# Optimization experiments

Hardware: AMD Instinct MI355X
Metric: run time of the kernel (lower is better)

The kernel has to match this reference:

```python
import jax, jax.numpy as jnp
import numpy as np

DIM = 768
HEADS = 12
HEAD_DIM = DIM // HEADS
SCALE = HEAD_DIM ** (-0.5)


def setup_inputs() -> dict:
    key = jax.random.key(0)
    k1, k2, k3, k4 = jax.random.split(key, 4)
    B, N = 2, 48 * 48
    x = jax.random.normal(k1, (B, N, DIM), dtype=jnp.float32)
    qkv_w = jax.random.normal(k2, (3 * DIM, DIM), dtype=jnp.float32) * (DIM ** -0.5)
    proj_w = jax.random.normal(k3, (DIM, DIM), dtype=jnp.float32) * (DIM ** -0.5)
    proj_b = jax.random.normal(k4, (DIM,), dtype=jnp.float32) * 0.02
    return {"x": x, "H": 48, "W": 48, "qkv_w": qkv_w, "proj_w": proj_w, "proj_b": proj_b}


def reference(x, H, W, qkv_w, proj_w, proj_b):
    B, N, C = x.shape
    h, d = HEADS, HEAD_DIM
    # qkv linear (no bias): [B,N,3C], then split into per-head q,k,v [B,h,N,d]
    qkv = jnp.einsum('bnc,fc->bnf', x, qkv_w)
    qkv = qkv.reshape(B, N, 3, h, d).transpose(2, 0, 3, 1, 4)
    q, k, v = qkv[0], qkv[1], qkv[2]
    attn = jnp.einsum('bhnd,bhmd->bhnm', q, k) * SCALE  # [B,h,N,N]
    attn = jax.nn.softmax(attn, axis=-1)
    out = jnp.einsum('bhnm,bhmd->bhnd', attn, v)  # [B,h,N,d]
    out = out.transpose(0, 2, 1, 3).reshape(B, N, C)
    out = jnp.einsum('bnc,fc->bnf', out, proj_w) + proj_b
    return out
```

## Files before the change

kernel.cpp:

```cpp
#include <hip/hip_runtime.h>

#define B_    2
#define N_    2304
#define C_    768
#define HEADS 12
#define D_    64
#define F3    2304
#define M_    (B_*N_)
#define SPLITS 2
#define KSPAN (N_/SPLITS)
#define QSCALE 0.18033688011112042f

typedef __attribute__((ext_vector_type(8)))  short bfrag;
typedef __attribute__((ext_vector_type(4)))  float ffrag;
typedef __attribute__((ext_vector_type(16))) float ffrag16;
typedef __attribute__((ext_vector_type(4)))  unsigned ufrag;
typedef __attribute__((ext_vector_type(2)))  unsigned uint2v;

__device__ __forceinline__ short f2bf(float f) {
    unsigned u = __float_as_uint(f);
    u += 0x7fff + ((u >> 16) & 1);
    return (short)(u >> 16);
}

__device__ __forceinline__ void gl2lds16(const void* g, void* l) {
    __builtin_amdgcn_global_load_lds(
        (const __attribute__((address_space(1))) void*)g,
        (__attribute__((address_space(3))) void*)l, 16, 0, 0);
}

__device__ __forceinline__ void wait_vm8() { asm volatile("s_waitcnt vmcnt(8)" ::: "memory"); }
__device__ __forceinline__ void wait_vm4() { asm volatile("s_waitcnt vmcnt(4)" ::: "memory"); }
__device__ __forceinline__ void wait_vm0() { asm volatile("s_waitcnt vmcnt(0)" ::: "memory"); }

__device__ __forceinline__ unsigned pktrunc(float a, float b) {
    return __builtin_amdgcn_perm(__float_as_uint(a), __float_as_uint(b),
                                 0x03020706u);
}

__global__ __launch_bounds__(256) void cast_all(const float* __restrict__ x,
                                                const float* __restrict__ qw,
                                                const float* __restrict__ pw,
                                                short* __restrict__ dst) {
    const int nx4 = (M_*C_)/4, nq4 = (F3*C_)/4, np4 = (C_*C_)/4;
    int i = blockIdx.x * 256 + threadIdx.x;
    if (i >= nx4 + nq4 + np4) return;
    const float* src; int off;
    if (i < nx4)            { src = x;  off = i; }
    else if (i < nx4 + nq4) { src = qw; off = i - nx4; }
    else                    { src = pw; off = i - nx4 - nq4; }
    float4 v = ((const float4*)src)[off];
    short4 o;
    o.x = f2bf(v.x); o.y = f2bf(v.y); o.z = f2bf(v.z); o.w = f2bf(v.w);
    ((short4*)dst)[i] = o;
}

__global__ __launch_bounds__(256) void qkv_gemm(const short* __restrict__ xb,
                                                const short* __restrict__ wb,
                                                short* __restrict__ Qb,
                                                short* __restrict__ Kb,
                                                short* __restrict__ Vtb) {
    __shared__ short As[3][128*32];
    __shared__ short Bs[3][128*32];
    const int t = threadIdx.x;
    const int w = t >> 6, lane = t & 63;
    const int quad = lane >> 4, l15 = lane & 15;
    const int wr = w >> 1, wc = w & 1;

    const int nwg = gridDim.x * gridDim.y;
    const int bid = blockIdx.y * gridDim.x + blockIdx.x;
    const int swz = (bid & 7) * (nwg >> 3) + (bid >> 3);
    const int m0 = (swz / gridDim.x) * 128, f0 = (swz % gridDim.x) * 128;

    const int srow = lane >> 2;
    const int skk  = (lane & 3) * 8;

    ffrag acc[4][4] = {};

    #pragma unroll
    for (int r = 0; r < 2; ++r) {
        int seg = r*4 + w;
        int row = seg*16 + srow;
        gl2lds16(xb + (size_t)(m0+row)*C_ + skk, As[0] + seg*512);
        gl2lds16(wb + (size_t)(f0+row)*C_ + skk, Bs[0] + seg*512);
    }
    #pragma unroll
    for (int r = 0; r < 2; ++r) {
        int seg = r*4 + w;
        int row = seg*16 + srow;
        gl2lds16(xb + (size_t)(m0+row)*C_ + 32 + skk, As[1] + seg*512);
        gl2lds16(wb + (size_t)(f0+row)*C_ + 32 + skk, Bs[1] + seg*512);
    }

    const int NKT = C_/32;
    int cur = 0;
    for (int kt = 0; kt < NKT; ++kt) {
        int pf = cur + 2; if (pf >= 3) pf -= 3;
        if (kt + 2 < NKT) {
            const int k0n = (kt+2)*32;
            #pragma unroll
            for (int r = 0; r < 2; ++r) {
                int seg = r*4 + w;
                int row = seg*16 + srow;
                gl2lds16(xb + (size_t)(m0+row)*C_ + k0n + skk, As[pf] + seg*512);
                gl2lds16(wb + (size_t)(f0+row)*C_ + k0n + skk, Bs[pf] + seg*512);
            }
            wait_vm8();
        } else if (kt + 1 < NKT) {
            wait_vm4();
        } else {
            wait_vm0();
        }
        __builtin_amdgcn_s_barrier();

        bfrag af[4], bf[4];
        #pragma unroll
        for (int i = 0; i < 4; ++i)
            af[i] = *(const bfrag*)(As[cur] + (wr*64 + i*16 + l15)*32 + quad*8);
        #pragma unroll
        for (int j = 0; j < 4; ++j)
            bf[j] = *(const bfrag*)(Bs[cur] + (wc*64 + j*16 + l15)*32 + quad*8);
        #pragma unroll
        for (int i = 0; i < 4; ++i)
            #pragma unroll
            for (int j = 0; j < 4; ++j)
                acc[i][j] = __builtin_amdgcn_mfma_f32_16x16x32_bf16(af[i], bf[j], acc[i][j], 0, 0, 0);
        __builtin_amdgcn_s_barrier();
        cur = cur + 1; if (cur >= 3) cur = 0;
    }

    const int b   = m0 / N_;
    const int seg = f0 + wc*64;
    const int which = seg / C_;
    const int head  = (seg - which*C_) >> 6;
    const int bh    = b*HEADS + head;
    const int nbase = (m0 - b*N_) + wr*64 + quad*4;

    if (which == 0) {
        #pragma unroll
        for (int i = 0; i < 4; ++i) {
            int n0 = nbase + i*16;
            #pragma unroll
            for (int j = 0; j < 4; ++j) {
                int d = j*16 + l15;
                #pragma unroll
                for (int r = 0; r < 4; ++r)
                    Qb[((size_t)bh*N_ + n0 + r)*D_ + d] = f2bf(acc[i][j][r] * QSCALE);
            }
        }
    } else if (which == 1) {
        #pragma unroll
        for (int i = 0; i < 4; ++i) {
            int n0 = nbase + i*16;
            #pragma unroll
            for (int j = 0; j < 4; ++j) {
                int d = j*16 + l15;
                #pragma unroll
                for (int r = 0; r < 4; ++r)
                    Kb[((size_t)bh*N_ + n0 + r)*D_ + d] = f2bf(acc[i][j][r]);
            }
        }
    } else {
        #pragma unroll
        for (int i = 0; i < 4; ++i) {
            int n0 = nbase + i*16;
            #pragma unroll
            for (int j = 0; j < 4; ++j) {
                int d = j*16 + l15;
                short4 vv;
                vv.x = f2bf(acc[i][j][0]);
                vv.y = f2bf(acc[i][j][1]);
                vv.z = f2bf(acc[i][j][2]);
                vv.w = f2bf(acc[i][j][3]);
                *(short4*)(Vtb + ((size_t)bh*D_ + d)*N_ + n0) = vv;
            }
        }
    }
}


__device__ __forceinline__ void qkpack(const short* Kc, const bfrag* qf,
                                       int kt, int l31, int hi,
                                       ufrag& u0, ufrag& u1) {
    ffrag16 s;
    #pragma unroll
    for (int r = 0; r < 16; ++r) s[r] = 0.f;
    int row = kt*32 + l31, r7 = row & 7;
    __builtin_amdgcn_s_setprio(1);
    #pragma unroll
    for (int kc = 0; kc < 4; ++kc) {
        bfrag kf = *(const bfrag*)(Kc + row*64 + ((kc*2 + hi) ^ r7)*8);
        s = __builtin_amdgcn_mfma_f32_32x32x16_bf16(kf, qf[kc], s, 0, 0, 0);
    }
    __builtin_amdgcn_s_setprio(0);
    #pragma unroll
    for (int r = 0; r < 16; ++r)
        s[r] = __builtin_amdgcn_exp2f(s[r]);
    unsigned q01_0 = pktrunc(s[0],  s[1]),  q23_0 = pktrunc(s[2],  s[3]);
    unsigned q01_1 = pktrunc(s[4],  s[5]),  q23_1 = pktrunc(s[6],  s[7]);
    unsigned q01_2 = pktrunc(s[8],  s[9]),  q23_2 = pktrunc(s[10], s[11]);
    unsigned q01_3 = pktrunc(s[12], s[13]), q23_3 = pktrunc(s[14], s[15]);
    uint2v e0 = __builtin_amdgcn_permlane32_swap(q01_0, q01_1, false, false);
    uint2v e1 = __builtin_amdgcn_permlane32_swap(q23_0, q23_1, false, false);
    uint2v e2 = __builtin_amdgcn_permlane32_swap(q01_2, q01_3, false, false);
    uint2v e3 = __builtin_amdgcn_permlane32_swap(q23_2, q23_3, false, false);
    ufrag lo, hif;
    lo[0]  = e0[0]; lo[1]  = e1[0]; lo[2]  = e0[1]; lo[3]  = e1[1];
    hif[0] = e2[0]; hif[1] = e3[0]; hif[2] = e2[1]; hif[3] = e3[1];
    u0 = lo; u1 = hif;
}

__device__ __forceinline__ void pv_lds(ufrag u0, ufrag u1, const short* Vc,
                                       int kt, int l31, int hi, bfrag vones,
                                       ffrag16& o0, ffrag16& o1, ffrag16& lf) {
    int r0 = l31, r7a = r0 & 7;
    int r1 = 32 + l31, r7b = r1 & 7;
    bfrag p0 = __builtin_bit_cast(bfrag, u0);
    bfrag p1 = __builtin_bit_cast(bfrag, u1);
    int kcA = kt*2, kcB = kt*2 + 1;
    bfrag vA0 = *(const bfrag*)(Vc + r0*64 + ((kcA*2 + hi) ^ r7a)*8);
    bfrag vA1 = *(const bfrag*)(Vc + r1*64 + ((kcA*2 + hi) ^ r7b)*8);
    bfrag vB0 = *(const bfrag*)(Vc + r0*64 + ((kcB*2 + hi) ^ r7a)*8);
    bfrag vB1 = *(const bfrag*)(Vc + r1*64 + ((kcB*2 + hi) ^ r7b)*8);
    o0 = __builtin_amdgcn_mfma_f32_32x32x16_bf16(p0, vA0, o0, 0, 0, 0);
    o1 = __builtin_amdgcn_mfma_f32_32x32x16_bf16(p0, vA1, o1, 0, 0, 0);
    lf = __builtin_amdgcn_mfma_f32_32x32x16_bf16(p0, vones, lf, 0, 0, 0);
    o0 = __builtin_amdgcn_mfma_f32_32x32x16_bf16(p1, vB0, o0, 0, 0, 0);
    o1 = __builtin_amdgcn_mfma_f32_32x32x16_bf16(p1, vB1, o1, 0, 0, 0);
    lf = __builtin_amdgcn_mfma_f32_32x32x16_bf16(p1, vones, lf, 0, 0, 0);
}

__device__ __forceinline__ void pv_reg(ufrag u0, ufrag u1,
                                       bfrag v0, bfrag v1, bfrag v2, bfrag v3,
                                       bfrag vones,
                                       ffrag16& o0, ffrag16& o1, ffrag16& lf) {
    bfrag p0 = __builtin_bit_cast(bfrag, u0);
    bfrag p1 = __builtin_bit_cast(bfrag, u1);
    o0 = __builtin_amdgcn_mfma_f32_32x32x16_bf16(p0, v0, o0, 0, 0, 0);
    o1 = __builtin_amdgcn_mfma_f32_32x32x16_bf16(p0, v1, o1, 0, 0, 0);
    lf = __builtin_amdgcn_mfma_f32_32x32x16_bf16(p0, vones, lf, 0, 0, 0);
    o0 = __builtin_amdgcn_mfma_f32_32x32x16_bf16(p1, v2, o0, 0, 0, 0);
    o1 = __builtin_amdgcn_mfma_f32_32x32x16_bf16(p1, v3, o1, 0, 0, 0);
    lf = __builtin_amdgcn_mfma_f32_32x32x16_bf16(p1, vones, lf, 0, 0, 0);
}

__device__ __forceinline__ void vload4(const short* Vc, int kt, int l31, int hi,
                                       bfrag& v0, bfrag& v1, bfrag& v2, bfrag& v3) {
    int r0 = l31, r7a = r0 & 7;
    int r1 = 32 + l31, r7b = r1 & 7;
    int kcA = kt*2, kcB = kt*2 + 1;
    v0 = *(const bfrag*)(Vc + r0*64 + ((kcA*2 + hi) ^ r7a)*8);
    v1 = *(const bfrag*)(Vc + r1*64 + ((kcA*2 + hi) ^ r7b)*8);
    v2 = *(const bfrag*)(Vc + r0*64 + ((kcB*2 + hi) ^ r7a)*8);
    v3 = *(const bfrag*)(Vc + r1*64 + ((kcB*2 + hi) ^ r7b)*8);
}

__global__ __launch_bounds__(256, 4) void attn_mfma(const short* __restrict__ Qb,
                                                    const short* __restrict__ Kb,
                                                    const short* __restrict__ Vtb,
                                                    float* __restrict__ Opart,
                                                    float* __restrict__ lpart) {
    __shared__ short lds[16384];
    const int t = threadIdx.x;
    const int w = t >> 6, lane = t & 63;
    const int l31 = lane & 31, hi = lane >> 5;

    const int nwg = gridDim.x * gridDim.y;
    const int fid = blockIdx.y * gridDim.x + blockIdx.x;
    const int swz = (fid & 7) * (nwg >> 3) + (fid >> 3);
    const int bh  = swz / gridDim.x;
    const int q0  = (swz - bh * gridDim.x) * 128;

    const int split = blockIdx.z;
    const int kbase = split * KSPAN;
    const size_t base = (size_t)bh * N_ * D_;
    const int lrow = lane >> 3;
    const int lc   = (lane & 7) ^ lrow;

    short* Qs = lds + 8192;

    #pragma unroll
    for (int r = 0; r < 4; ++r) {
        int s = r*4 + w;
        gl2lds16(Qb + base + (size_t)(q0 + s*8 + lrow)*D_ + lc*8, Qs + s*512);
    }
    #pragma unroll
    for (int r = 0; r < 2; ++r) {
        int s = r*4 + w;
        int row = s*8 + lrow;
        gl2lds16(Kb  + base + (size_t)(kbase+row)*D_ + lc*8,    lds + s*512);
        gl2lds16(Vtb + (size_t)(bh*D_ + row)*N_ + kbase + lc*8, lds + 4096 + s*512);
    }
    __syncthreads();

    bfrag qf[4];
    {
        int row = w*32 + l31, r7 = row & 7;
        #pragma unroll
        for (int kc = 0; kc < 4; ++kc)
            qf[kc] = *(const bfrag*)(Qs + row*64 + ((kc*2 + hi) ^ r7)*8);
    }
    __syncthreads();

    bfrag vones;
    #pragma unroll
    for (int j = 0; j < 8; ++j) vones[j] = (short)0x3f80;

    ffrag16 oacc0, oacc1, lfr;
    #pragma unroll
    for (int r = 0; r < 16; ++r) { oacc0[r] = 0.f; oacc1[r] = 0.f; lfr[r] = 0.f; }

    const int NT = KSPAN / 64;

    ufrag pP0, pP1;
    bfrag vP0, vP1, vP2, vP3;

    {
        const int k0n = kbase + 64;
        #pragma unroll
        for (int r = 0; r < 2; ++r) {
            int s = r*4 + w;
            int row = s*8 + lrow;
            gl2lds16(Kb  + base + (size_t)(k0n+row)*D_ + lc*8,    lds + 8192 + s*512);
            gl2lds16(Vtb + (size_t)(bh*D_ + row)*N_ + k0n + lc*8, lds + 12288 + s*512);
        }
        const short* Kc = lds;
        const short* Vc = lds + 4096;
        ufrag a0, a1;
        qkpack(Kc, qf, 0, l31, hi, a0, a1);
        __builtin_amdgcn_s_setprio(1);
        pv_lds(a0, a1, Vc, 0, l31, hi, vones, oacc0, oacc1, lfr);
        __builtin_amdgcn_s_setprio(0);
        qkpack(Kc, qf, 1, l31, hi, pP0, pP1);
        vload4(Vc, 1, l31, hi, vP0, vP1, vP2, vP3);
        __builtin_amdgcn_s_barrier();
    }

    for (int ti = 1; ti < NT; ++ti) {
        const int cur = ti & 1;
        const short* Kc = lds + cur*8192;
        const short* Vc = Kc + 4096;

        if (ti + 1 < NT) {
            short* Kn = lds + (cur^1)*8192;
            const int k0n = kbase + (ti+1)*64;
            #pragma unroll
            for (int r = 0; r < 2; ++r) {
                int s = r*4 + w;
                int row = s*8 + lrow;
                gl2lds16(Kb  + base + (size_t)(k0n+row)*D_ + lc*8,    Kn + s*512);
                gl2lds16(Vtb + (size_t)(bh*D_ + row)*N_ + k0n + lc*8, Kn + 4096 + s*512);
            }
            wait_vm4();
        } else {
            wait_vm0();
        }
        __builtin_amdgcn_s_barrier();

        ufrag a0, a1;
        qkpack(Kc, qf, 0, l31, hi, a0, a1);
        __builtin_amdgcn_s_setprio(1);
        pv_reg(pP0, pP1, vP0, vP1, vP2, vP3, vones, oacc0, oacc1, lfr);
        pv_lds(a0, a1, Vc, 0, l31, hi, vones, oacc0, oacc1, lfr);
        __builtin_amdgcn_s_setprio(0);
        qkpack(Kc, qf, 1, l31, hi, pP0, pP1);
        vload4(Vc, 1, l31, hi, vP0, vP1, vP2, vP3);
        __builtin_amdgcn_s_barrier();
    }

    pv_reg(pP0, pP1, vP0, vP1, vP2, vP3, vones, oacc0, oacc1, lfr);

    const int b = bh / HEADS, head = bh - b*HEADS;
    float* Op = Opart + (size_t)split * M_ * C_;
    float* lp = lpart + (size_t)split * (B_*HEADS) * N_;

    if (l31 == 0) {
        #pragma unroll
        for (int r = 0; r < 16; ++r) {
            int n = q0 + w*32 + (r & 3) + 8*(r >> 2) + 4*hi;
            lp[bh*N_ + n] = lfr[r];
        }
    }

    #pragma unroll
    for (int r = 0; r < 16; ++r) {
        int n = q0 + w*32 + (r & 3) + 8*(r >> 2) + 4*hi;
        int c = head*D_ + l31;
        Op[((size_t)b*N_ + n)*C_ + c] = oacc0[r];
        Op[((size_t)b*N_ + n)*C_ + c + 32] = oacc1[r];
    }
}

__global__ __launch_bounds__(256) void attn_merge(const float* __restrict__ Opart,
                                                  const float* __restrict__ lpart,
                                                  short* __restrict__ Ob) {
    int i = blockIdx.x * 256 + threadIdx.x;
    int m = i / (C_/4);
    int c = (i - m*(C_/4)) * 4;
    int b = m / N_, n = m - b*N_;
    int bh = b*HEADS + (c >> 6);
    float4 o0 = ((const float4*)Opart)[i];
    float4 o1 = ((const float4*)(Opart + (size_t)M_*C_))[i];
    float l = lpart[bh*N_ + n] + lpart[(B_*HEADS)*N_ + bh*N_ + n];
    float inv = 1.f / l;
    short4 o;
    o.x = f2bf((o0.x + o1.x) * inv);
    o.y = f2bf((o0.y + o1.y) * inv);
    o.z = f2bf((o0.z + o1.z) * inv);
    o.w = f2bf((o0.w + o1.w) * inv);
    ((short4*)Ob)[i] = o;
}

__global__ __launch_bounds__(256) void proj_gemm(const short* __restrict__ Ab,
                                                 const short* __restrict__ wb,
                                                 const float* __restrict__ bias,
                                                 float* __restrict__ out) {
    __shared__ short As[3][128*32];
    __shared__ short Bs[3][128*32];
    const int t = threadIdx.x;
    const int w = t >> 6, lane = t & 63;
    const int quad = lane >> 4, l15 = lane & 15;
    const int wr = w >> 1, wc = w & 1;

    const int nwg = gridDim.x * gridDim.y;
    const int bid = blockIdx.y * gridDim.x + blockIdx.x;
    const int swz = (bid & 7) * (nwg >> 3) + (bid >> 3);
    const int m0 = (swz / gridDim.x) * 128, f0 = (swz % gridDim.x) * 128;

    const int srow = lane >> 2;
    const int skk  = (lane & 3) * 8;

    ffrag acc[4][4] = {};

    #pragma unroll
    for (int r = 0; r < 2; ++r) {
        int seg = r*4 + w;
        int row = seg*16 + srow;
        gl2lds16(Ab + (size_t)(m0+row)*C_ + skk, As[0] + seg*512);
        gl2lds16(wb + (size_t)(f0+row)*C_ + skk, Bs[0] + seg*512);
    }
    #pragma unroll
    for (int r = 0; r < 2; ++r) {
        int seg = r*4 + w;
        int row = seg*16 + srow;
        gl2lds16(Ab + (size_t)(m0+row)*C_ + 32 + skk, As[1] + seg*512);
        gl2lds16(wb + (size_t)(f0+row)*C_ + 32 + skk, Bs[1] + seg*512);
    }

    const int NKT = C_/32;
    int cur = 0;
    for (int kt = 0; kt < NKT; ++kt) {
        int pf = cur + 2; if (pf >= 3) pf -= 3;
        if (kt + 2 < NKT) {
            const int k0n = (kt+2)*32;
            #pragma unroll
            for (int r = 0; r < 2; ++r) {
                int seg = r*4 + w;
                int row = seg*16 + srow;
                gl2lds16(Ab + (size_t)(m0+row)*C_ + k0n + skk, As[pf] + seg*512);
                gl2lds16(wb + (size_t)(f0+row)*C_ + k0n + skk, Bs[pf] + seg*512);
            }
            wait_vm8();
        } else if (kt + 1 < NKT) {
            wait_vm4();
        } else {
            wait_vm0();
        }
        __builtin_amdgcn_s_barrier();

        bfrag af[4], bf[4];
        #pragma unroll
        for (int i = 0; i < 4; ++i)
            af[i] = *(const bfrag*)(As[cur] + (wr*64 + i*16 + l15)*32 + quad*8);
        #pragma unroll
        for (int j = 0; j < 4; ++j)
            bf[j] = *(const bfrag*)(Bs[cur] + (wc*64 + j*16 + l15)*32 + quad*8);
        #pragma unroll
        for (int i = 0; i < 4; ++i)
            #pragma unroll
            for (int j = 0; j < 4; ++j)
                acc[i][j] = __builtin_amdgcn_mfma_f32_16x16x32_bf16(af[i], bf[j], acc[i][j], 0, 0, 0);
        __builtin_amdgcn_s_barrier();
        cur = cur + 1; if (cur >= 3) cur = 0;
    }

    #pragma unroll
    for (int i = 0; i < 4; ++i) {
        int mbase = m0 + wr*64 + i*16 + quad*4;
        #pragma unroll
        for (int j = 0; j < 4; ++j) {
            int f = f0 + wc*64 + j*16 + l15;
            float bv = bias[f];
            #pragma unroll
            for (int r = 0; r < 4; ++r)
                out[(size_t)(mbase + r)*C_ + f] = acc[i][j][r] + bv;
        }
    }
}

extern "C" void kernel_launch(void* const* d_in, const int* in_sizes, int n_in,
                              void* d_out, int out_size, void* d_ws, size_t ws_size,
                              hipStream_t stream) {
    const float* x      = (const float*)d_in[0];
    const float* qkv_w  = (const float*)d_in[3];
    const float* proj_w = (const float*)d_in[4];
    const float* proj_b = (const float*)d_in[5];
    float* out = (float*)d_out;

    const size_t nx = (size_t)M_ * C_;
    const size_t nq = (size_t)F3 * C_;
    const size_t np = (size_t)C_ * C_;
    short* xb  = (short*)d_ws;
    short* qwb = xb  + nx;
    short* pwb = qwb + nq;
    short* Qb  = pwb + np;
    short* Kb  = Qb  + nx;
    short* Vtb = Kb  + nx;
    short* Ob  = Vtb + nx;
    float* Opart = (float*)(Ob + nx);
    float* lpart = Opart + (size_t)SPLITS * M_ * C_;

    const int ncast4 = (int)((nx + nq + np) / 4);
    cast_all<<<dim3((ncast4 + 255)/256), 256, 0, stream>>>(x, qkv_w, proj_w, xb);

    qkv_gemm<<<dim3(F3/128, M_/128), 256, 0, stream>>>(xb, qwb, Qb, Kb, Vtb);
    attn_mfma<<<dim3(N_/128, B_*HEADS, SPLITS), 256, 0, stream>>>(Qb, Kb, Vtb, Opart, lpart);
    attn_merge<<<dim3(((int)(nx/4) + 255)/256), 256, 0, stream>>>(Opart, lpart, Ob);
    proj_gemm<<<dim3(C_/128, M_/128), 256, 0, stream>>>(Ob, pwb, proj_b, out);
}
```

Measured before the change: 192.4 us.

## Fuse attention split-merge into projection GEMM A-tile loading

Removes the separate attn_merge kernel and has proj_gemm read the two fp32 partial attention outputs and row sums directly. It combines them, normalizes, converts to bf16 and writes the A tile into shared memory. This saves one launch and a bf16 round trip through global memory. In exchange the A operand is now read as fp32 from both splits by every column block (6 blocks per row tile), the pipeline drops from triple to double buffering, and register-staged loads add extra barriers each k-step.

New measurement: 204.7 us. 1.06x slower.

```diff
diff --git a/kernel.cpp b/kernel.cpp
--- a/kernel.cpp
+++ b/kernel.cpp
@@ -32,6 +32,7 @@
 __device__ __forceinline__ void wait_vm8() { asm volatile("s_waitcnt vmcnt(8)" ::: "memory"); }
 __device__ __forceinline__ void wait_vm4() { asm volatile("s_waitcnt vmcnt(4)" ::: "memory"); }
 __device__ __forceinline__ void wait_vm0() { asm volatile("s_waitcnt vmcnt(0)" ::: "memory"); }
+__device__ __forceinline__ void wait_lgkm0() { asm volatile("s_waitcnt lgkmcnt(0)" ::: "memory"); }
 
 __device__ __forceinline__ unsigned pktrunc(float a, float b) {
     return __builtin_amdgcn_perm(__float_as_uint(a), __float_as_uint(b),
@@ -391,32 +392,13 @@
     }
 }
 
-__global__ __launch_bounds__(256) void attn_merge(const float* __restrict__ Opart,
-                                                  const float* __restrict__ lpart,
-                                                  short* __restrict__ Ob) {
-    int i = blockIdx.x * 256 + threadIdx.x;
-    int m = i / (C_/4);
-    int c = (i - m*(C_/4)) * 4;
-    int b = m / N_, n = m - b*N_;
-    int bh = b*HEADS + (c >> 6);
-    float4 o0 = ((const float4*)Opart)[i];
-    float4 o1 = ((const float4*)(Opart + (size_t)M_*C_))[i];
-    float l = lpart[bh*N_ + n] + lpart[(B_*HEADS)*N_ + bh*N_ + n];
-    float inv = 1.f / l;
-    short4 o;
-    o.x = f2bf((o0.x + o1.x) * inv);
-    o.y = f2bf((o0.y + o1.y) * inv);
-    o.z = f2bf((o0.z + o1.z) * inv);
-    o.w = f2bf((o0.w + o1.w) * inv);
-    ((short4*)Ob)[i] = o;
-}
-
-__global__ __launch_bounds__(256) void proj_gemm(const short* __restrict__ Ab,
+__global__ __launch_bounds__(256) void proj_gemm(const float* __restrict__ Opart,
+                                                 const float* __restrict__ lpart,
                                                  const short* __restrict__ wb,
                                                  const float* __restrict__ bias,
                                                  float* __restrict__ out) {
-    __shared__ short As[3][128*32];
-    __shared__ short Bs[3][128*32];
+    __shared__ short As[2][128*32];
+    __shared__ short Bs[2][128*32];
     const int t = threadIdx.x;
     const int w = t >> 6, lane = t & 63;
     const int quad = lane >> 4, l15 = lane & 15;
@@ -430,43 +412,73 @@
     const int srow = lane >> 2;
     const int skk  = (lane & 3) * 8;
 
+    const int b = m0 / N_;
+    const int LP = (B_*HEADS) * N_;
+    const size_t MC = (size_t)M_ * C_;
+
     ffrag acc[4][4] = {};
 
-    #pragma unroll
-    for (int r = 0; r < 2; ++r) {
-        int seg = r*4 + w;
-        int row = seg*16 + srow;
-        gl2lds16(Ab + (size_t)(m0+row)*C_ + skk, As[0] + seg*512);
-        gl2lds16(wb + (size_t)(f0+row)*C_ + skk, Bs[0] + seg*512);
-    }
-    #pragma unroll
-    for (int r = 0; r < 2; ++r) {
-        int seg = r*4 + w;
-        int row = seg*16 + srow;
-        gl2lds16(Ab + (size_t)(m0+row)*C_ + 32 + skk, As[1] + seg*512);
-        gl2lds16(wb + (size_t)(f0+row)*C_ + 32 + skk, Bs[1] + seg*512);
-    }
+    float4 pa[2][2], pb[2][2];
+    float lv[2];
+
+    auto issueA = [&](int kt) {
+        const int gcol = kt*32 + skk;
+        const int bh = b*HEADS + (kt >> 1);
+        #pragma unroll
+        for (int r = 0; r < 2; ++r) {
+            int seg = r*4 + w;
+            int row = seg*16 + srow;
+            int m = m0 + row;
+            int n = m - b*N_;
+            const float* p0 = Opart + (size_t)m*C_ + gcol;
+            pa[r][0] = *(const float4*)p0;
+            pa[r][1] = *(const float4*)(p0 + 4);
+            const float* p1 = p0 + MC;
+            pb[r][0] = *(const float4*)p1;
+            pb[r][1] = *(const float4*)(p1 + 4);
+            lv[r] = lpart[bh*N_ + n] + lpart[LP + bh*N_ + n];
+        }
+    };
+    auto writeA = [&](int buf) {
+        #pragma unroll
+        for (int r = 0; r < 2; ++r) {
+            int seg = r*4 + w;
+            float inv = 1.f / lv[r];
+            bfrag o;
+            o[0] = f2bf((pa[r][0].x + pb[r][0].x) * inv);
+            o[1] = f2bf((pa[r][0].y + pb[r][0].y) * inv);
+            o[2] = f2bf((pa[r][0].z + pb[r][0].z) * inv);
+            o[3] = f2bf((pa[r][0].w + pb[r][0].w) * inv);
+            o[4] = f2bf((pa[r][1].x + pb[r][1].x) * inv);
+            o[5] = f2bf((pa[r][1].y + pb[r][1].y) * inv);
+            o[6] = f2bf((pa[r][1].z + pb[r][1].z) * inv);
+            o[7] = f2bf((pa[r][1].w + pb[r][1].w) * inv);
+            *(bfrag*)(As[buf] + seg*512 + lane*8) = o;
+        }
+    };
+    auto issueB = [&](int kt, int buf) {
+        const int k0n = kt*32;
+        #pragma unroll
+        for (int r = 0; r < 2; ++r) {
+            int seg = r*4 + w;
+            int row = seg*16 + srow;
+            gl2lds16(wb + (size_t)(f0+row)*C_ + k0n + skk, Bs[buf] + seg*512);
+        }
+    };
+
+    issueB(0, 0);
+    issueA(0);
+    wait_vm0();
+    writeA(0);
+    __syncthreads();
 
     const int NKT = C_/32;
-    int cur = 0;
     for (int kt = 0; kt < NKT; ++kt) {
-        int pf = cur + 2; if (pf >= 3) pf -= 3;
-        if (kt + 2 < NKT) {
-            const int k0n = (kt+2)*32;
-            #pragma unroll
-            for (int r = 0; r < 2; ++r) {
-                int seg = r*4 + w;
-                int row = seg*16 + srow;
-                gl2lds16(Ab + (size_t)(m0+row)*C_ + k0n + skk, As[pf] + seg*512);
-                gl2lds16(wb + (size_t)(f0+row)*C_ + k0n + skk, Bs[pf] + seg*512);
-            }
-            wait_vm8();
-        } else if (kt + 1 < NKT) {
-            wait_vm4();
-        } else {
-            wait_vm0();
-        }
-        __builtin_amdgcn_s_barrier();
+        const int cur = kt & 1;
+        if (kt + 1 < NKT) {
+            issueB(kt + 1, cur ^ 1);
+            issueA(kt + 1);
+        }
 
         bfrag af[4], bf[4];
         #pragma unroll
@@ -480,8 +492,14 @@
             #pragma unroll
             for (int j = 0; j < 4; ++j)
                 acc[i][j] = __builtin_amdgcn_mfma_f32_16x16x32_bf16(af[i], bf[j], acc[i][j], 0, 0, 0);
-        __builtin_amdgcn_s_barrier();
-        cur = cur + 1; if (cur >= 3) cur = 0;
+
+        if (kt + 1 < NKT) {
+            __builtin_amdgcn_s_barrier();
+            wait_vm0();
+            writeA(cur ^ 1);
+            wait_lgkm0();
+            __builtin_amdgcn_s_barrier();
+        }
     }
 
     #pragma unroll
@@ -525,6 +543,5 @@
 
     qkv_gemm<<<dim3(F3/128, M_/128), 256, 0, stream>>>(xb, qwb, Qb, Kb, Vtb);
     attn_mfma<<<dim3(N_/128, B_*HEADS, SPLITS), 256, 0, stream>>>(Qb, Kb, Vtb, Opart, lpart);
-    attn_merge<<<dim3(((int)(nx/4) + 255)/256), 256, 0, stream>>>(Opart, lpart, Ob);
-    proj_gemm<<<dim3(C_/128, M_/128), 256, 0, stream>>>(Ob, pwb, proj_b, out);
-}
+    proj_gemm<<<dim3(C_/128, M_/128), 256, 0, stream>>>(Opart, lpart, pwb, proj_b, out);
+}
```

## Fuse split-K attention merge into attention kernel via atomic last-block counter

Applied to the files above, without the earlier changes.

Drops the separate attn_merge launch. Each attention workgroup now atomically increments a per-tile counter after writing its partial output, and the last split to finish merges both partials, normalises, and writes the bf16 output for that tile. This removes one kernel launch and gives the merge a chance to read partials while they are still cache-resident. The cost is a threadfence, an atomic, and a serial tail of merge work inside the attention kernel. The counters are zeroed inside cast_all.

After: 343.9 us. 1.79x slower.

```diff
diff --git a/kernel.cpp b/kernel.cpp
--- a/kernel.cpp
+++ b/kernel.cpp
@@ -9,6 +9,8 @@
 #define M_    (B_*N_)
 #define SPLITS 2
 #define KSPAN (N_/SPLITS)
+#define NQT   (N_/128)
+#define NTILES (B_*HEADS*NQT)
 #define QSCALE 0.18033688011112042f
 
 typedef __attribute__((ext_vector_type(8)))  short bfrag;
@@ -41,7 +43,11 @@
 __global__ __launch_bounds__(256) void cast_all(const float* __restrict__ x,
                                                 const float* __restrict__ qw,
                                                 const float* __restrict__ pw,
-                                                short* __restrict__ dst) {
+                                                short* __restrict__ dst,
+                                                int* __restrict__ cnt) {
+    if (blockIdx.x == 0) {
+        for (int z = threadIdx.x; z < NTILES; z += 256) cnt[z] = 0;
+    }
     const int nx4 = (M_*C_)/4, nq4 = (F3*C_)/4, np4 = (C_*C_)/4;
     int i = blockIdx.x * 256 + threadIdx.x;
     if (i >= nx4 + nq4 + np4) return;
@@ -259,8 +265,11 @@
                                                     const short* __restrict__ Kb,
                                                     const short* __restrict__ Vtb,
                                                     float* __restrict__ Opart,
-                                                    float* __restrict__ lpart) {
+                                                    float* __restrict__ lpart,
+                                                    short* __restrict__ Ob,
+                                                    int* __restrict__ cnt) {
     __shared__ short lds[16384];
+    __shared__ int winner;
     const int t = threadIdx.x;
     const int w = t >> 6, lane = t & 63;
     const int l31 = lane & 31, hi = lane >> 5;
@@ -269,7 +278,8 @@
     const int fid = blockIdx.y * gridDim.x + blockIdx.x;
     const int swz = (fid & 7) * (nwg >> 3) + (fid >> 3);
     const int bh  = swz / gridDim.x;
-    const int q0  = (swz - bh * gridDim.x) * 128;
+    const int qt  = swz - bh * gridDim.x;
+    const int q0  = qt * 128;
 
     const int split = blockIdx.z;
     const int kbase = split * KSPAN;
@@ -389,26 +399,37 @@
         Op[((size_t)b*N_ + n)*C_ + c] = oacc0[r];
         Op[((size_t)b*N_ + n)*C_ + c + 32] = oacc1[r];
     }
-}
-
-__global__ __launch_bounds__(256) void attn_merge(const float* __restrict__ Opart,
-                                                  const float* __restrict__ lpart,
-                                                  short* __restrict__ Ob) {
-    int i = blockIdx.x * 256 + threadIdx.x;
-    int m = i / (C_/4);
-    int c = (i - m*(C_/4)) * 4;
-    int b = m / N_, n = m - b*N_;
-    int bh = b*HEADS + (c >> 6);
-    float4 o0 = ((const float4*)Opart)[i];
-    float4 o1 = ((const float4*)(Opart + (size_t)M_*C_))[i];
-    float l = lpart[bh*N_ + n] + lpart[(B_*HEADS)*N_ + bh*N_ + n];
-    float inv = 1.f / l;
-    short4 o;
-    o.x = f2bf((o0.x + o1.x) * inv);
-    o.y = f2bf((o0.y + o1.y) * inv);
-    o.z = f2bf((o0.z + o1.z) * inv);
-    o.w = f2bf((o0.w + o1.w) * inv);
-    ((short4*)Ob)[i] = o;
+
+    __threadfence();
+    if (t == 0) {
+        int old = atomicAdd(&cnt[bh * NQT + qt], 1);
+        winner = (old == SPLITS - 1);
+    }
+    __syncthreads();
+    if (winner) {
+        __threadfence();
+        const float* O0 = Opart;
+        const float* O1 = Opart + (size_t)M_ * C_;
+        const float* l0 = lpart;
+        const float* l1 = lpart + (size_t)(B_*HEADS) * N_;
+        #pragma unroll
+        for (int k = 0; k < 8; ++k) {
+            int v = k*256 + t;
+            int row = v >> 4, c4 = v & 15;
+            int n = q0 + row;
+            float l = l0[bh*N_ + n] + l1[bh*N_ + n];
+            float inv = 1.f / l;
+            size_t off = ((size_t)b*N_ + n)*C_ + head*D_ + c4*4;
+            float4 a = *(const float4*)(O0 + off);
+            float4 bb = *(const float4*)(O1 + off);
+            short4 o;
+            o.x = f2bf((a.x + bb.x) * inv);
+            o.y = f2bf((a.y + bb.y) * inv);
+            o.z = f2bf((a.z + bb.z) * inv);
+            o.w = f2bf((a.w + bb.w) * inv);
+            *(short4*)(Ob + off) = o;
+        }
+    }
 }
 
 __global__ __launch_bounds__(256) void proj_gemm(const short* __restrict__ Ab,
@@ -519,12 +540,12 @@
     short* Ob  = Vtb + nx;
     float* Opart = (float*)(Ob + nx);
     float* lpart = Opart + (size_t)SPLITS * M_ * C_;
+    int*   cnt   = (int*)(lpart + (size_t)SPLITS * (B_*HEADS) * N_);
 
     const int ncast4 = (int)((nx + nq + np) / 4);
-    cast_all<<<dim3((ncast4 + 255)/256), 256, 0, stream>>>(x, qkv_w, proj_w, xb);
+    cast_all<<<dim3((ncast4 + 255)/256), 256, 0, stream>>>(x, qkv_w, proj_w, xb, cnt);
 
     qkv_gemm<<<dim3(F3/128, M_/128), 256, 0, stream>>>(xb, qwb, Qb, Kb, Vtb);
-    attn_mfma<<<dim3(N_/128, B_*HEADS, SPLITS), 256, 0, stream>>>(Qb, Kb, Vtb, Opart, lpart);
-    attn_merge<<<dim3(((int)(nx/4) + 255)/256), 256, 0, stream>>>(Opart, lpart, Ob);
+    attn_mfma<<<dim3(NQT, B_*HEADS, SPLITS), 256, 0, stream>>>(Qb, Kb, Vtb, Opart, lpart, Ob, cnt);
     proj_gemm<<<dim3(C_/128, M_/128), 256, 0, stream>>>(Ob, pwb, proj_b, out);
 }
```
